# Kernel tuning notes

Measured on AMD Instinct MI355X. Metric: run time of the kernel, lower is better.

## Reference

```python
import jax, jax.numpy as jnp
import numpy as np

N_NODES = 100000
N_EDGES = 3200000
H, D = 3, 12  # heads, per-head dim; H*D == node_hidden_dim == 36
NEG_SLOPE = 0.2


def setup_inputs() -> dict:
    key = jax.random.key(0)
    ks = jax.random.split(key, 11)
    s = 0.1
    return {
        "node_features": jax.random.normal(ks[0], (N_NODES, 36), jnp.float32),
        "src": jax.random.randint(ks[1], (N_EDGES,), 0, N_NODES),
        "dst": jax.random.randint(ks[2], (N_EDGES,), 0, N_NODES),
        "lin0_w": jax.random.normal(ks[3], (36, 36), jnp.float32) * s,
        "lin0_b": jax.random.normal(ks[4], (36,), jnp.float32) * s,
        "fc_w": jax.random.normal(ks[5], (3, 36, 36), jnp.float32) * s,
        "attn_l": jax.random.normal(ks[6], (3, H, D), jnp.float32) * s,
        "attn_r": jax.random.normal(ks[7], (3, H, D), jnp.float32) * s,
        "gat_bias": jax.random.normal(ks[8], (3, 36), jnp.float32) * s,
        "out_w": jax.random.normal(ks[9], (36, 36), jnp.float32) * s,
        "out_b": jax.random.normal(ks[10], (36,), jnp.float32) * s,
    }


def _gat_layer(h, src, dst, fc_w, a_l, a_r, bias):
    n = h.shape[0]
    feat = (h @ fc_w).reshape(n, H, D)                      # (N,H,D)
    el = jnp.sum(feat * a_l, axis=-1)                       # (N,H)
    er = jnp.sum(feat * a_r, axis=-1)                       # (N,H)
    e = el[src] + er[dst]                                   # (E,H)
    e = jnp.where(e >= 0, e, NEG_SLOPE * e)                 # leaky_relu(0.2)
    # edge softmax over incoming edges of each dst node (numerically stable)
    m = jax.ops.segment_max(e, dst, num_segments=n)         # (N,H)
    m = jnp.where(jnp.isfinite(m), m, 0.0)                  # zero-degree guard
    ee = jnp.exp(e - m[dst])                                # (E,H)
    denom = jax.ops.segment_sum(ee, dst, num_segments=n)    # (N,H)
    alpha = ee / jnp.maximum(denom[dst], 1e-9)              # (E,H)
    msg = feat[src] * alpha[:, :, None]                     # (E,H,D)
    rst = jax.ops.segment_sum(msg, dst, num_segments=n)     # (N,H,D)
    # residual (Identity since in_feats == H*D) + bias, then ELU
    rst = rst + h.reshape(n, H, D) + bias.reshape(1, H, D)
    return jax.nn.elu(rst).reshape(n, H * D)


def reference(node_features, src, dst, lin0_w, lin0_b, fc_w, attn_l, attn_r, gat_bias, out_w, out_b):
    h = node_features @ lin0_w + lin0_b
    for l in range(3):
        h = _gat_layer(h, src, dst, fc_w[l], attn_l[l], attn_r[l], gat_bias[l])
    return h @ out_w + out_b
```

## Files before the change

### kernel.cpp

```cpp
#include <hip/hip_runtime.h>
#include <math.h>

#define HID 36
#define NH 3
#define HD 12
#define PROW 64
#define BSHIFT 13
#define NBUCK 13
#define PSHIFT 8
#define PCHUNK 2048
#define SPCAP 9216
#define CSRCAP 4096
#define NSTEP 8

typedef _Float16 f16;


__global__ void __launch_bounds__(256, 1)
lin0_hist_kernel(const float* __restrict__ x, const float* __restrict__ w0,
                 const float* __restrict__ b0, const float* __restrict__ fcw,
                 const float* __restrict__ al, const float* __restrict__ ar,
                 float* __restrict__ h, f16* __restrict__ packed,
                 float* __restrict__ er, int n, int nb_lin,
                 const int* __restrict__ dst, int* __restrict__ M, int E, int C,
                 int np) {
    int t = threadIdx.x;
    if ((int)blockIdx.x >= nb_lin) {
        __shared__ int hcnt[512];
        int c = blockIdx.x - nb_lin;
        for (int i = t; i < 512; i += 256) hcnt[i] = 0;
        __syncthreads();
        int i0 = c * PCHUNK;
        int i1 = min(i0 + PCHUNK, E);
        for (int i = i0 + t; i < i1; i += 256)
            atomicAdd(&hcnt[dst[i] >> PSHIFT], 1);
        __syncthreads();
        for (int b = t; b < np; b += 256)
            M[(size_t)b * C + c] = hcnt[b];
        return;
    }
    __shared__ float W0[HID * HID];
    __shared__ float W1[HID * HID];
    __shared__ float Bs[HID], ALs[HID], ARs[HID];
    for (int i = t; i < HID * HID; i += 256) { W0[i] = w0[i]; W1[i] = fcw[i]; }
    if (t < HID) { Bs[t] = b0[t]; ALs[t] = al[t]; ARs[t] = ar[t]; }
    __syncthreads();
    int node = blockIdx.x * 256 + t;
    if (node >= n) return;
    const float4* xp = (const float4*)(x + (size_t)node * HID);
    float h0[HID];
#pragma unroll
    for (int j = 0; j < HID; ++j) h0[j] = Bs[j];
#pragma unroll
    for (int kk = 0; kk < HID / 4; ++kk) {
        float4 xv = xp[kk];
        const float* w = &W0[(4 * kk) * HID];
#pragma unroll
        for (int j = 0; j < HID; ++j)
            h0[j] += xv.x * w[j] + xv.y * w[HID + j] + xv.z * w[2 * HID + j] + xv.w * w[3 * HID + j];
    }
    float* hp = h + (size_t)node * HID;
#pragma unroll
    for (int j = 0; j < HID; ++j) hp[j] = h0[j];
    float feat[HID];
#pragma unroll
    for (int j = 0; j < HID; ++j) feat[j] = 0.f;
#pragma unroll
    for (int k = 0; k < HID; ++k) {
        float hv = h0[k];
        const float* w = &W1[k * HID];
#pragma unroll
        for (int j = 0; j < HID; ++j) feat[j] += hv * w[j];
    }
    union { f16 hx[48]; uint4 q[6]; } u;
#pragma unroll
    for (int hh = 0; hh < NH; ++hh) {
        float sl = 0.f, sr = 0.f;
#pragma unroll
        for (int d = 0; d < HD; ++d) {
            sl += feat[hh * HD + d] * ALs[hh * HD + d];
            sr += feat[hh * HD + d] * ARs[hh * HD + d];
        }
#pragma unroll
        for (int d = 0; d < HD; ++d) u.hx[hh * 16 + d] = (f16)feat[hh * HD + d];
        u.hx[hh * 16 + 12] = (f16)sl;
        u.hx[hh * 16 + 13] = (f16)0.f;
        u.hx[hh * 16 + 14] = (f16)0.f;
        u.hx[hh * 16 + 15] = (f16)0.f;
        er[node * NH + hh] = sr;
    }
    uint4* prow = (uint4*)(packed + (size_t)node * PROW);
#pragma unroll
    for (int q = 0; q < 6; ++q) prow[q] = u.q[q];
}

__global__ void base_scan_kernel(const int* __restrict__ M, int* __restrict__ BaseT,
                                 int* __restrict__ T, int C, int np) {
    __shared__ int tmp[512];
    int b = blockIdx.x;
    int t = threadIdx.x;
    int carry = 0;
    for (int base = 0; base < C; base += 512) {
        int idx = base + t;
        int v = (idx < C) ? M[(size_t)b * C + idx] : 0;
        tmp[t] = v;
        __syncthreads();
        for (int ofs = 1; ofs < 512; ofs <<= 1) {
            int x = 0;
            if (t >= ofs) x = tmp[t - ofs];
            __syncthreads();
            tmp[t] += x;
            __syncthreads();
        }
        if (idx < C) BaseT[(size_t)idx * 512 + b] = carry + tmp[t] - v;
        carry += tmp[511];
        __syncthreads();
    }
    if (t == 0) T[b] = carry;
}

__global__ void part_scatter_kernel(const int* __restrict__ src, const int* __restrict__ dst,
                                    const int* __restrict__ BaseT, const int* __restrict__ T,
                                    int* __restrict__ part, int E, int np) {
    __shared__ int h[512];
    __shared__ int tsc[512];
    __shared__ int base[512];
    int t = threadIdx.x;
    int c = blockIdx.x;
    int v = (t < np) ? T[t] : 0;
    tsc[t] = v;
    h[t] = 0;
    __syncthreads();
    for (int ofs = 1; ofs < 512; ofs <<= 1) {
        int x = 0;
        if (t >= ofs) x = tsc[t - ofs];
        __syncthreads();
        tsc[t] += x;
        __syncthreads();
    }
    if (t < np) base[t] = (tsc[t] - v) + BaseT[(size_t)c * 512 + t];
    __syncthreads();
    int i0 = c * PCHUNK;
    int i1 = min(i0 + PCHUNK, E);
    for (int i = i0 + t; i < i1; i += blockDim.x) {
        int d = dst[i];
        int bin = d >> PSHIFT;
        int r = atomicAdd(&h[bin], 1);
        part[base[bin] + r] = (src[i] << PSHIFT) | (d & ((1 << PSHIFT) - 1));
    }
}

__global__ void bucket_csr_kernel(const int* __restrict__ part, const int* __restrict__ T,
                                  int* __restrict__ csr, int* __restrict__ off,
                                  int n, int E, int np) {
    __shared__ int cnt[256 * NBUCK];
    __shared__ int psum[512];
    __shared__ int smpart[SPCAP];
    __shared__ int e0s;
    int p = blockIdx.x;
    int t = threadIdx.x;
    int v = (t < np) ? T[t] : 0;
    psum[t] = v;
    __syncthreads();
    for (int ofs = 1; ofs < 512; ofs <<= 1) {
        int x = 0;
        if (t >= ofs) x = psum[t - ofs];
        __syncthreads();
        psum[t] += x;
        __syncthreads();
    }
    if (t == p) e0s = psum[t] - v;
    __syncthreads();
    int e0 = e0s;
    int dbase = p << PSHIFT;
    int nd = min(256, n - dbase);
    int nc = nd * NBUCK;
    for (int i = t; i < nc; i += blockDim.x) cnt[i] = 0;
    __syncthreads();
    int cnt_p = T[p];
    const int* pp = part + e0;
    bool fits = (cnt_p <= SPCAP);
    for (int i = t; i < cnt_p; i += blockDim.x) {
        int e = pp[i];
        if (fits) smpart[i] = e;
        atomicAdd(&cnt[(e & 255) * NBUCK + ((e >> PSHIFT) >> BSHIFT)], 1);
    }
    __syncthreads();
    int sum = 0;
    if (t < nd) {
        for (int k = 0; k < NBUCK; ++k) {
            int c = cnt[t * NBUCK + k];
            cnt[t * NBUCK + k] = sum;
            sum += c;
        }
    }
    psum[t] = (t < nd) ? sum : 0;
    __syncthreads();
    for (int ofs = 1; ofs < 512; ofs <<= 1) {
        int x = 0;
        if (t >= ofs) x = psum[t - ofs];
        __syncthreads();
        psum[t] += x;
        __syncthreads();
    }
    int dexcl = (t > 0) ? psum[t - 1] : 0;
    int start = e0 + dexcl;
    if (t < nd) {
        for (int k = 0; k < NBUCK; ++k) cnt[t * NBUCK + k] += start;
        off[dbase + t] = start;
    }
    __syncthreads();
    for (int i = t; i < cnt_p; i += blockDim.x) {
        int e = fits ? smpart[i] : pp[i];
        int s = e >> PSHIFT;
        int idx = (e & 255) * NBUCK + (s >> BSHIFT);
        int pos = atomicAdd(&cnt[idx], 1);
        csr[pos] = s << 6;
    }
    if (p == 0 && t == 0) off[n] = E;
}


__device__ __forceinline__ void edge_accum(uint4 qa, uint4 qb, float ern,
                                           float& denom, float* acc) {
    union { uint4 q[2]; f16 hx[16]; } v;
    v.q[0] = qa;
    v.q[1] = qb;
    float e = (float)v.hx[12] + ern;
    e = (e >= 0.f) ? e : 0.2f * e;
    float w = __expf(e);
    denom += w;
#pragma unroll
    for (int k = 0; k < HD; ++k) acc[k] += w * (float)v.hx[k];
}

template <bool FITS>
__device__ __forceinline__ void sweep_paced(const int* __restrict__ smbuf,
                                            const int* __restrict__ csre,
                                            int j0, int deg, const f16* __restrict__ pb,
                                            float ern, float& denom, float* acc) {
    int j = j0;
#pragma unroll 1
    for (int s2 = 1; s2 <= NSTEP; ++s2) {
        int jend = j0 + ((deg * s2) >> 3);
        int c = jend - j;
        for (; c >= 4; c -= 4, j += 4) {
            int o0 = FITS ? smbuf[j]     : csre[j];
            int o1 = FITS ? smbuf[j + 1] : csre[j + 1];
            int o2 = FITS ? smbuf[j + 2] : csre[j + 2];
            int o3 = FITS ? smbuf[j + 3] : csre[j + 3];
            const uint4* r0 = (const uint4*)(pb + o0);
            const uint4* r1 = (const uint4*)(pb + o1);
            const uint4* r2 = (const uint4*)(pb + o2);
            const uint4* r3 = (const uint4*)(pb + o3);
            uint4 a0 = r0[0], b0 = r0[1];
            uint4 a1 = r1[0], b1 = r1[1];
            uint4 a2 = r2[0], b2 = r2[1];
            uint4 a3 = r3[0], b3 = r3[1];
            edge_accum(a0, b0, ern, denom, acc);
            edge_accum(a1, b1, ern, denom, acc);
            edge_accum(a2, b2, ern, denom, acc);
            edge_accum(a3, b3, ern, denom, acc);
        }
        for (; c > 0; --c, ++j) {
            int o = FITS ? smbuf[j] : csre[j];
            const uint4* r = (const uint4*)(pb + o);
            edge_accum(r[0], r[1], ern, denom, acc);
        }
    }
}

__global__ void __launch_bounds__(192)
aggtr_kernel(const f16* __restrict__ packed_in, const float* __restrict__ er_in,
             const float* __restrict__ hcur,
             const int* __restrict__ off, const int* __restrict__ csr,
             const float* __restrict__ bias, const float* __restrict__ wnext,
             const float* __restrict__ aln, const float* __restrict__ arn,
             float* __restrict__ hnext, f16* __restrict__ packed_out,
             float* __restrict__ er_out, int n) {
    __shared__ float Wsh[HID * HID];
    __shared__ float ALs[HID], ARs[HID];
    __shared__ int smbuf[CSRCAP];
    int t = threadIdx.x;
    for (int i = t; i < HID * HID; i += 192) Wsh[i] = wnext[i];
    if (t < HID) { ALs[t] = aln[t]; ARs[t] = arn[t]; }
    int ln = t / 3, hh = t - ln * 3;
    int nb0 = blockIdx.x * 64;
    int node = nb0 + ln;
    bool active = (node < n);

    int e0 = off[nb0];
    int e1 = off[min(nb0 + 64, n)];
    int span = e1 - e0;
    bool fits = (span <= CSRCAP);
    if (fits)
        for (int i = t; i < span; i += 192) smbuf[i] = csr[e0 + i];

    int j0 = 0, deg = 0;
    float ern = 0.f;
    if (active) {
        j0 = off[node] - e0;
        deg = off[node + 1] - e0 - j0;
        ern = er_in[node * NH + hh];
    }
    const f16* pb = packed_in + hh * 16;
    const int* csre = csr + e0;
    __syncthreads();

    float denom = 0.f;
    float acc[HD];
#pragma unroll
    for (int k = 0; k < HD; ++k) acc[k] = 0.f;

    if (fits) sweep_paced<true>(smbuf, csre, j0, deg, pb, ern, denom, acc);
    else      sweep_paced<false>(smbuf, csre, j0, deg, pb, ern, denom, acc);
    __syncthreads();

    float* hsh = (float*)smbuf;
    float v[HD];
#pragma unroll
    for (int k = 0; k < HD; ++k) v[k] = 0.f;
    if (active) {
        float inv = 1.f / fmaxf(denom, 1e-9f);
        int base = node * HID + hh * HD;
        const float4* hc = (const float4*)(hcur + base);
        float4 h0 = hc[0], h1 = hc[1], h2 = hc[2];
        float hres[HD] = {h0.x, h0.y, h0.z, h0.w, h1.x, h1.y, h1.z, h1.w, h2.x, h2.y, h2.z, h2.w};
#pragma unroll
        for (int k = 0; k < HD; ++k) {
            float x = acc[k] * inv + hres[k] + bias[hh * HD + k];
            v[k] = (x > 0.f) ? x : expm1f(x);
        }
        float4* hp = (float4*)(hnext + base);
        hp[0] = make_float4(v[0], v[1], v[2], v[3]);
        hp[1] = make_float4(v[4], v[5], v[6], v[7]);
        hp[2] = make_float4(v[8], v[9], v[10], v[11]);
    }
#pragma unroll
    for (int k = 0; k < HD; ++k) hsh[ln * 37 + hh * HD + k] = v[k];
    __syncthreads();

    float feat[HD];
#pragma unroll
    for (int d = 0; d < HD; ++d) feat[d] = 0.f;
    const float* hrow = &hsh[ln * 37];
#pragma unroll 4
    for (int k = 0; k < HID; ++k) {
        float hv = hrow[k];
        const float* w = &Wsh[k * HID + hh * HD];
#pragma unroll
        for (int d = 0; d < HD; ++d) feat[d] += hv * w[d];
    }
    if (!active) return;
    float sl = 0.f, sr = 0.f;
#pragma unroll
    for (int d = 0; d < HD; ++d) {
        sl += feat[d] * ALs[hh * HD + d];
        sr += feat[d] * ARs[hh * HD + d];
    }
    union { f16 hx[16]; uint4 q[2]; } o;
#pragma unroll
    for (int d = 0; d < HD; ++d) o.hx[d] = (f16)feat[d];
    o.hx[12] = (f16)sl;
    o.hx[13] = (f16)0.f; o.hx[14] = (f16)0.f; o.hx[15] = (f16)0.f;
    uint4* prow = (uint4*)(packed_out + (size_t)node * PROW + hh * 16);
    prow[0] = o.q[0];
    prow[1] = o.q[1];
    er_out[node * NH + hh] = sr;
}

__global__ void __launch_bounds__(192)
aggout_kernel(const f16* __restrict__ packed_in, const float* __restrict__ er_in,
              const float* __restrict__ hcur,
              const int* __restrict__ off, const int* __restrict__ csr,
              const float* __restrict__ bias, const float* __restrict__ ow,
              const float* __restrict__ ob, float* __restrict__ out, int n) {
    __shared__ float Wsh[HID * HID];
    __shared__ float OBs[HID];
    __shared__ int smbuf[CSRCAP];
    int t = threadIdx.x;
    for (int i = t; i < HID * HID; i += 192) Wsh[i] = ow[i];
    if (t < HID) OBs[t] = ob[t];
    int ln = t / 3, hh = t - ln * 3;
    int nb0 = blockIdx.x * 64;
    int node = nb0 + ln;
    bool active = (node < n);

    int e0 = off[nb0];
    int e1 = off[min(nb0 + 64, n)];
    int span = e1 - e0;
    bool fits = (span <= CSRCAP);
    if (fits)
        for (int i = t; i < span; i += 192) smbuf[i] = csr[e0 + i];

    int j0 = 0, deg = 0;
    float ern = 0.f;
    if (active) {
        j0 = off[node] - e0;
        deg = off[node + 1] - e0 - j0;
        ern = er_in[node * NH + hh];
    }
    const f16* pb = packed_in + hh * 16;
    const int* csre = csr + e0;
    __syncthreads();

    float denom = 0.f;
    float acc[HD];
#pragma unroll
    for (int k = 0; k < HD; ++k) acc[k] = 0.f;

    if (fits) sweep_paced<true>(smbuf, csre, j0, deg, pb, ern, denom, acc);
    else      sweep_paced<false>(smbuf, csre, j0, deg, pb, ern, denom, acc);
    __syncthreads();

    float* hsh = (float*)smbuf;
    float v[HD];
#pragma unroll
    for (int k = 0; k < HD; ++k) v[k] = 0.f;
    if (active) {
        float inv = 1.f / fmaxf(denom, 1e-9f);
        int base = node * HID + hh * HD;
        const float4* hc = (const float4*)(hcur + base);
        float4 h0 = hc[0], h1 = hc[1], h2 = hc[2];
        float hres[HD] = {h0.x, h0.y, h0.z, h0.w, h1.x, h1.y, h1.z, h1.w, h2.x, h2.y, h2.z, h2.w};
#pragma unroll
        for (int k = 0; k < HD; ++k) {
            float x = acc[k] * inv + hres[k] + bias[hh * HD + k];
            v[k] = (x > 0.f) ? x : expm1f(x);
        }
    }
#pragma unroll
    for (int k = 0; k < HD; ++k) hsh[ln * 37 + hh * HD + k] = v[k];
    __syncthreads();

    float feat[HD];
#pragma unroll
    for (int d = 0; d < HD; ++d) feat[d] = OBs[hh * HD + d];
    const float* hrow = &hsh[ln * 37];
#pragma unroll 4
    for (int k = 0; k < HID; ++k) {
        float hv = hrow[k];
        const float* w = &Wsh[k * HID + hh * HD];
#pragma unroll
        for (int d = 0; d < HD; ++d) feat[d] += hv * w[d];
    }
    if (!active) return;
    float4* op = (float4*)(out + (size_t)node * HID + hh * HD);
    op[0] = make_float4(feat[0], feat[1], feat[2], feat[3]);
    op[1] = make_float4(feat[4], feat[5], feat[6], feat[7]);
    op[2] = make_float4(feat[8], feat[9], feat[10], feat[11]);
}


extern "C" void kernel_launch(void* const* d_in, const int* in_sizes, int n_in,
                              void* d_out, int out_size, void* d_ws, size_t ws_size,
                              hipStream_t stream) {
    const float* xnf = (const float*)d_in[0];
    const int* src = (const int*)d_in[1];
    const int* dst = (const int*)d_in[2];
    const float* l0w = (const float*)d_in[3];
    const float* l0b = (const float*)d_in[4];
    const float* fcw = (const float*)d_in[5];
    const float* al  = (const float*)d_in[6];
    const float* ar  = (const float*)d_in[7];
    const float* gb  = (const float*)d_in[8];
    const float* ow  = (const float*)d_in[9];
    const float* ob  = (const float*)d_in[10];
    float* out = (float*)d_out;
    const int N = in_sizes[0] / HID;
    const int E = in_sizes[1];
    const int NP = (N + (1 << PSHIFT) - 1) >> PSHIFT;
    const int C = (E + PCHUNK - 1) / PCHUNK;

    char* p = (char*)d_ws;
    auto alloc = [&](size_t bytes) {
        char* r = p;
        p += (bytes + 255) & ~(size_t)255;
        return r;
    };
    int* part    = (int*)alloc((size_t)E * 4);
    int* M       = (int*)alloc((size_t)NP * C * 4);
    int* BaseT   = (int*)alloc((size_t)C * 512 * 4);
    int* T       = (int*)alloc((size_t)NP * 4);
    int* off     = (int*)alloc((size_t)(N + 1) * 4);
    int* csr     = (int*)alloc((size_t)E * 4);
    float* ha    = (float*)alloc((size_t)N * HID * 4);
    float* hb    = (float*)alloc((size_t)N * HID * 4);
    f16* pkA     = (f16*)alloc((size_t)N * PROW * 2);
    f16* pkB     = (f16*)alloc((size_t)N * PROW * 2);
    float* erA   = (float*)alloc((size_t)N * NH * 4);
    float* erB   = (float*)alloc((size_t)N * NH * 4);

    int nblk = (N + 255) / 256;
    int fblk = (N + 63) / 64;

    lin0_hist_kernel<<<nblk + C, 256, 0, stream>>>(xnf, l0w, l0b, fcw, al, ar,
                                                   ha, pkA, erA, N, nblk,
                                                   dst, M, E, C, NP);
    base_scan_kernel<<<NP, 512, 0, stream>>>(M, BaseT, T, C, NP);
    part_scatter_kernel<<<C, 512, 0, stream>>>(src, dst, BaseT, T, part, E, NP);
    bucket_csr_kernel<<<NP, 512, 0, stream>>>(part, T, csr, off, N, E, NP);

    aggtr_kernel<<<fblk, 192, 0, stream>>>(pkA, erA, ha, off, csr, gb,
                                           fcw + (size_t)1 * HID * HID, al + HID, ar + HID,
                                           hb, pkB, erB, N);
    aggtr_kernel<<<fblk, 192, 0, stream>>>(pkB, erB, hb, off, csr, gb + HID,
                                           fcw + (size_t)2 * HID * HID, al + 2 * HID, ar + 2 * HID,
                                           ha, pkA, erA, N);
    aggout_kernel<<<fblk, 192, 0, stream>>>(pkA, erA, ha, off, csr, gb + 2 * HID,
                                            ow, ob, out, N);
}
```

Baseline: 367.9 us.

## Stage partition scatter and CSR bucket writes through shared memory

The partition scatter kernel now sorts each chunk's edges by destination bin in shared memory, so the global writes to the partition array become contiguous runs per bin instead of scattered stores. The bucket CSR kernel builds its output in a shared buffer and copies it to global memory coalesced, and it rereads the partition array from global instead of caching it. This targets uncoalesced global writes in CSR construction, at the cost of more LDS usage (lower occupancy), extra barriers and an added local prefix scan.

```diff
diff --git a/kernel.cpp b/kernel.cpp
--- a/kernel.cpp
+++ b/kernel.cpp
@@ -122,14 +122,19 @@
 __global__ void part_scatter_kernel(const int* __restrict__ src, const int* __restrict__ dst,
                                     const int* __restrict__ BaseT, const int* __restrict__ T,
                                     int* __restrict__ part, int E, int np) {
-    __shared__ int h[512];
     __shared__ int tsc[512];
     __shared__ int base[512];
+    __shared__ int hexcl[512];
+    __shared__ int hcur[512];
+    __shared__ int smsrc[PCHUNK];
+    __shared__ int smdst[PCHUNK];
+    __shared__ int smsort[PCHUNK];
+    __shared__ short smbin[PCHUNK];
     int t = threadIdx.x;
     int c = blockIdx.x;
     int v = (t < np) ? T[t] : 0;
     tsc[t] = v;
-    h[t] = 0;
+    hcur[t] = 0;
     __syncthreads();
     for (int ofs = 1; ofs < 512; ofs <<= 1) {
         int x = 0;
@@ -141,12 +146,38 @@
     if (t < np) base[t] = (tsc[t] - v) + BaseT[(size_t)c * 512 + t];
     __syncthreads();
     int i0 = c * PCHUNK;
-    int i1 = min(i0 + PCHUNK, E);
-    for (int i = i0 + t; i < i1; i += blockDim.x) {
-        int d = dst[i];
+    int cnum = min(i0 + PCHUNK, E) - i0;
+    for (int i = t; i < cnum; i += 512) {
+        int s = src[i0 + i], d = dst[i0 + i];
+        smsrc[i] = s;
+        smdst[i] = d;
+        atomicAdd(&hcur[d >> PSHIFT], 1);
+    }
+    __syncthreads();
+    int hv = hcur[t];
+    tsc[t] = hv;
+    __syncthreads();
+    for (int ofs = 1; ofs < 512; ofs <<= 1) {
+        int x = 0;
+        if (t >= ofs) x = tsc[t - ofs];
+        __syncthreads();
+        tsc[t] += x;
+        __syncthreads();
+    }
+    hexcl[t] = tsc[t] - hv;
+    hcur[t] = tsc[t] - hv;
+    __syncthreads();
+    for (int i = t; i < cnum; i += 512) {
+        int d = smdst[i];
         int bin = d >> PSHIFT;
-        int r = atomicAdd(&h[bin], 1);
-        part[base[bin] + r] = (src[i] << PSHIFT) | (d & ((1 << PSHIFT) - 1));
+        int pos = atomicAdd(&hcur[bin], 1);
+        smsort[pos] = (smsrc[i] << PSHIFT) | (d & ((1 << PSHIFT) - 1));
+        smbin[pos] = (short)bin;
+    }
+    __syncthreads();
+    for (int i = t; i < cnum; i += 512) {
+        int bin = smbin[i];
+        part[base[bin] + (i - hexcl[bin])] = smsort[i];
     }
 }
 
@@ -155,7 +186,7 @@
                                   int n, int E, int np) {
     __shared__ int cnt[256 * NBUCK];
     __shared__ int psum[512];
-    __shared__ int smpart[SPCAP];
+    __shared__ int smout[SPCAP];
     __shared__ int e0s;
     int p = blockIdx.x;
     int t = threadIdx.x;
@@ -182,7 +213,6 @@
     bool fits = (cnt_p <= SPCAP);
     for (int i = t; i < cnt_p; i += blockDim.x) {
         int e = pp[i];
-        if (fits) smpart[i] = e;
         atomicAdd(&cnt[(e & 255) * NBUCK + ((e >> PSHIFT) >> BSHIFT)], 1);
     }
     __syncthreads();
@@ -210,12 +240,25 @@
         off[dbase + t] = start;
     }
     __syncthreads();
-    for (int i = t; i < cnt_p; i += blockDim.x) {
-        int e = fits ? smpart[i] : pp[i];
-        int s = e >> PSHIFT;
-        int idx = (e & 255) * NBUCK + (s >> BSHIFT);
-        int pos = atomicAdd(&cnt[idx], 1);
-        csr[pos] = s << 6;
+    if (fits) {
+        for (int i = t; i < cnt_p; i += blockDim.x) {
+            int e = pp[i];
+            int s = e >> PSHIFT;
+            int idx = (e & 255) * NBUCK + (s >> BSHIFT);
+            int pos = atomicAdd(&cnt[idx], 1);
+            smout[pos - e0] = s << 6;
+        }
+        __syncthreads();
+        for (int i = t; i < cnt_p; i += blockDim.x)
+            csr[e0 + i] = smout[i];
+    } else {
+        for (int i = t; i < cnt_p; i += blockDim.x) {
+            int e = pp[i];
+            int s = e >> PSHIFT;
+            int idx = (e & 255) * NBUCK + (s >> BSHIFT);
+            int pos = atomicAdd(&cnt[idx], 1);
+            csr[pos] = s << 6;
+        }
     }
     if (p == 0 && t == 0) off[n] = E;
 }
```

Result: faster. 337.4 us (-8.3%).
